# Kernel tuning notes

Hardware: AMD Instinct MI355X
Metric: run time of the kernel (lower is better)

## Reference

```python
import jax, jax.numpy as jnp
import numpy as np

C = 256        # channel
C4 = C // 4    # q/k projection dim
B, NQ, NK = 2, 8192, 8192
BN_EPS = 1e-5


def setup_inputs() -> dict:
    key = jax.random.key(0)
    ks = jax.random.split(key, 8)
    q_tensor = jax.random.normal(ks[0], (B, NQ, C), dtype=jnp.float32)
    kv_tensor = jax.random.normal(ks[1], (B, NK, C), dtype=jnp.float32)
    # 1x1 Conv1d weights == linear layers over the channel dim
    wq = jax.random.normal(ks[2], (C4, C), dtype=jnp.float32) * 0.02
    wk = jax.random.normal(ks[3], (C4, C), dtype=jnp.float32) * 0.02
    wv = jax.random.normal(ks[4], (C, C), dtype=jnp.float32) * 0.02
    wt = jax.random.normal(ks[5], (C, C), dtype=jnp.float32) * 0.02
    bt = jnp.zeros((C,), dtype=jnp.float32)
    # BatchNorm1d (eval mode): affine params + running stats
    gamma = jax.random.uniform(ks[6], (C,), dtype=jnp.float32, minval=0.5, maxval=1.5)
    beta = jax.random.normal(ks[7], (C,), dtype=jnp.float32) * 0.1
    run_mean = jnp.zeros((C,), dtype=jnp.float32)
    run_var = jnp.ones((C,), dtype=jnp.float32)
    return {"q_tensor": q_tensor, "kv_tensor": kv_tensor, "wq": wq, "wk": wk,
            "wv": wv, "wt": wt, "bt": bt, "gamma": gamma, "beta": beta,
            "run_mean": run_mean, "run_var": run_var}


def reference(q_tensor, kv_tensor, wq, wk, wv, wt, bt, gamma, beta, run_mean, run_var):
    # 1x1 conv projections (channel-last form of Conv1d on permuted input)
    x_q = jnp.einsum('bnc,dc->bnd', q_tensor, wq)    # [B, NQ, C4]
    x_k = jnp.einsum('bnc,dc->bnd', kv_tensor, wk)   # [B, NK, C4]
    x_v = jnp.einsum('bnc,dc->bnd', kv_tensor, wv)   # [B, NK, C]
    # unscaled attention: matmul -> softmax -> matmul
    energy = jnp.einsum('bqd,bkd->bqk', x_q, x_k)    # [B, NQ, NK]
    attention = jax.nn.softmax(energy, axis=-1)
    x_r = jnp.einsum('bqk,bkc->bqc', attention, x_v)  # [B, NQ, C]
    # residual difference -> trans conv -> BN (eval) -> ReLU -> residual add
    res = q_tensor - x_r
    y = jnp.einsum('bnc,dc->bnd', res, wt) + bt
    y = (y - run_mean) * jax.lax.rsqrt(run_var + BN_EPS) * gamma + beta
    return jax.nn.relu(y) + q_tensor
```

## Files before the change

### kernel.cpp

```cpp
#include <hip/hip_runtime.h>
#include <hip/hip_bf16.h>

#define DEVINL __device__ __forceinline__

typedef short bf16x8 __attribute__((ext_vector_type(8)));
typedef float f32x4  __attribute__((ext_vector_type(4)));
typedef float f32x16 __attribute__((ext_vector_type(16)));
typedef unsigned int uint2v __attribute__((ext_vector_type(2)));

struct alignas(8) S4 { short x, y, z, w; };

DEVINL short f2bf(float f) {
  __hip_bfloat16 h = __float2bfloat16(f);
  short s; __builtin_memcpy(&s, &h, 2); return s;
}
DEVINL float bf2f(short s) {
  unsigned u = ((unsigned)(unsigned short)s) << 16;
  float f; __builtin_memcpy(&f, &u, 4); return f;
}

DEVINL f32x4 mfma16(bf16x8 a, bf16x8 b, f32x4 c) {
  return __builtin_amdgcn_mfma_f32_16x16x32_bf16(a, b, c, 0, 0, 0);
}
DEVINL f32x16 mfma32(bf16x8 a, bf16x8 b, f32x16 c) {
  return __builtin_amdgcn_mfma_f32_32x32x16_bf16(a, b, c, 0, 0, 0);
}

DEVINL void gld_lds16(const void* gptr, void* lptr) {
  __builtin_amdgcn_global_load_lds(
      (const __attribute__((address_space(1))) unsigned int*)gptr,
      (__attribute__((address_space(3))) unsigned int*)lptr, 16, 0, 0);
}

#define CC 256
#define C4 64
#define BB 2
#define NQ 8192
#define NK 8192
#define NROWS (BB * NQ)
#define DT 10.0f
#define LOG2E 1.44269504f

__global__ void k_setup(const float* __restrict__ wq, const float* __restrict__ wk,
                        const float* __restrict__ wv, const float* __restrict__ wt,
                        const float* __restrict__ bt, const float* __restrict__ gmm,
                        const float* __restrict__ bet, const float* __restrict__ rmean,
                        const float* __restrict__ rvar,
                        short* __restrict__ wqb, short* __restrict__ wkb,
                        short* __restrict__ wvb, short* __restrict__ wtb,
                        float* __restrict__ scale, float* __restrict__ bias) {
  int i = blockIdx.x * 256 + threadIdx.x;
  if (i < C4 * CC) { wqb[i] = f2bf(wq[i] * LOG2E); wkb[i] = f2bf(wk[i]); }
  if (i < CC * CC) { wvb[i] = f2bf(wv[i]); wtb[i] = f2bf(wt[i]); }
  if (i < CC) {
    float s = gmm[i] * rsqrtf(rvar[i] + 1e-5f);
    scale[i] = s;
    bias[i]  = (bt[i] - rmean[i]) * s + bet[i];
  }
}

__global__ __launch_bounds__(256)
void k_projqk(const float* __restrict__ q, const float* __restrict__ kv,
              const short* __restrict__ wqb, const short* __restrict__ wkb,
              short* __restrict__ xq, short* __restrict__ xk) {
  const float* A; const short* W; short* O;
  const bool swz = (blockIdx.y == 1);
  if (!swz) { A = q; W = wqb; O = xq; } else { A = kv; W = wkb; O = xk; }
  const int lane = threadIdx.x & 63, w = threadIdx.x >> 6;
  const int rowbase = blockIdx.x * 128 + w * 32;
  const int lr = lane & 15, lg = lane >> 4;
  f32x4 acc[2][4] = {};
#pragma unroll
  for (int kf = 0; kf < 8; ++kf) {
    bf16x8 a[2];
#pragma unroll
    for (int mf = 0; mf < 2; ++mf) {
      const float* p = A + (size_t)(rowbase + mf * 16 + lr) * CC + kf * 32 + lg * 8;
      float4 x0 = *(const float4*)p, x1 = *(const float4*)(p + 4);
      bf16x8 t;
      t[0] = f2bf(x0.x); t[1] = f2bf(x0.y); t[2] = f2bf(x0.z); t[3] = f2bf(x0.w);
      t[4] = f2bf(x1.x); t[5] = f2bf(x1.y); t[6] = f2bf(x1.z); t[7] = f2bf(x1.w);
      a[mf] = t;
    }
#pragma unroll
    for (int nf = 0; nf < 4; ++nf) {
      bf16x8 b = *(const bf16x8*)(W + (size_t)(nf * 16 + lr) * CC + kf * 32 + lg * 8);
      acc[0][nf] = mfma16(a[0], b, acc[0][nf]);
      acc[1][nf] = mfma16(a[1], b, acc[1][nf]);
    }
  }
#pragma unroll
  for (int mf = 0; mf < 2; ++mf)
#pragma unroll
    for (int nf = 0; nf < 4; ++nf)
#pragma unroll
      for (int r = 0; r < 4; ++r) {
        int row = rowbase + mf * 16 + lg * 4 + r;
        int d = nf * 16 + lr;
        int off = swz ? ((((d >> 3) ^ (row & 7)) << 3) + (d & 7)) : d;
        O[(size_t)row * C4 + off] = f2bf(acc[mf][nf][r]);
      }
}

__global__ __launch_bounds__(256)
void k_projv(const float* __restrict__ kv, const short* __restrict__ wvb,
             short* __restrict__ vt) {
  const int lane = threadIdx.x & 63, w = threadIdx.x >> 6;
  const int rowbase = blockIdx.x * 128 + w * 32;
  const int cb = blockIdx.y * 128;
  const int lr = lane & 15, lg = lane >> 4;
  f32x4 acc[2][8] = {};
#pragma unroll
  for (int kf = 0; kf < 8; ++kf) {
    bf16x8 a[2];
#pragma unroll
    for (int mf = 0; mf < 2; ++mf) {
      const float* p = kv + (size_t)(rowbase + mf * 16 + lr) * CC + kf * 32 + lg * 8;
      float4 x0 = *(const float4*)p, x1 = *(const float4*)(p + 4);
      bf16x8 t;
      t[0] = f2bf(x0.x); t[1] = f2bf(x0.y); t[2] = f2bf(x0.z); t[3] = f2bf(x0.w);
      t[4] = f2bf(x1.x); t[5] = f2bf(x1.y); t[6] = f2bf(x1.z); t[7] = f2bf(x1.w);
      a[mf] = t;
    }
#pragma unroll
    for (int nf = 0; nf < 8; ++nf) {
      bf16x8 b = *(const bf16x8*)(wvb + (size_t)(cb + nf * 16 + lr) * CC + kf * 32 + lg * 8);
      acc[0][nf] = mfma16(a[0], b, acc[0][nf]);
      acc[1][nf] = mfma16(a[1], b, acc[1][nf]);
    }
  }
#pragma unroll
  for (int mf = 0; mf < 2; ++mf) {
    int row = rowbase + mf * 16 + lg * 4;
    int bidx = row >> 13, kib = row & 8191;
    int tile = kib >> 6, kk = kib & 63;
#pragma unroll
    for (int nf = 0; nf < 8; ++nf) {
      int c = cb + nf * 16 + lr;
      S4 st;
      st.x = f2bf(acc[mf][nf][0]); st.y = f2bf(acc[mf][nf][1]);
      st.z = f2bf(acc[mf][nf][2]); st.w = f2bf(acc[mf][nf][3]);
      int off = (((kk >> 3) ^ (c & 7)) << 3) + (kk & 7);
      *(S4*)(vt + (((size_t)bidx * 128 + tile) * CC + c) * 64 + off) = st;
    }
  }
}

__global__ __launch_bounds__(256, 2)
void k_attn(const short* __restrict__ xq, const short* __restrict__ xk,
            const short* __restrict__ vt, float* __restrict__ xr,
            short* __restrict__ po, float* __restrict__ pm,
            float* __restrict__ pl, int nsplit) {
  __shared__ char Lds[40960];
  char* Kt = Lds;
  char* Vt = Lds + 8192;
  const int tid = threadIdx.x;
  const int ln = tid & 63, w = tid >> 6;
  const int qcol = ln & 31, hi = ln >> 5;
  const int b = blockIdx.y, qt = blockIdx.x, kz = blockIdx.z;
  const int kpb = (NK / 64) / nsplit;
  const int kt0 = kz * kpb, kt1 = kt0 + kpb;

  bf16x8 qb[4];
  {
    const short* qrow = xq + (size_t)(b * NQ + qt * 128 + w * 32 + qcol) * C4;
#pragma unroll
    for (int ds = 0; ds < 4; ++ds)
      qb[ds] = *(const bf16x8*)(qrow + ds * 16 + hi * 8);
  }
  f32x16 o[8] = {};
  float m = -1e30f, lsum = 0.f;

  const char* kgbase = (const char*)(xk + (size_t)b * NK * C4);
  const char* vgbase = (const char*)(vt + (size_t)b * 128 * 16384);

  auto stage = [&](int kt) {
    const char* ks = kgbase + (size_t)kt * 8192;
    const char* vs = vgbase + (size_t)kt * 32768;
#pragma unroll
    for (int i = 0; i < 2; ++i)
      gld_lds16(ks + (w * 2 + i) * 1024 + ln * 16, Kt + (w * 2 + i) * 1024);
#pragma unroll
    for (int i = 0; i < 8; ++i)
      gld_lds16(vs + (w * 8 + i) * 1024 + ln * 16, Vt + (w * 8 + i) * 1024);
  };

  stage(kt0);
#pragma unroll 1
  for (int kt = kt0; kt < kt1; ++kt) {
    __syncthreads();
    f32x16 s[2] = {};
#pragma unroll
    for (int kb = 0; kb < 2; ++kb) {
      int key = kb * 32 + qcol;
#pragma unroll
      for (int ds = 0; ds < 4; ++ds) {
        int cc = ds * 2 + hi;
        bf16x8 ka = *(const bf16x8*)(Kt + key * 128 + ((cc ^ (key & 7)) << 4));
        s[kb] = mfma32(ka, qb[ds], s[kb]);
      }
    }
    float pmax = s[0][0];
#pragma unroll
    for (int r = 1; r < 16; ++r) pmax = fmaxf(pmax, s[0][r]);
#pragma unroll
    for (int r = 0; r < 16; ++r) pmax = fmaxf(pmax, s[1][r]);
    pmax = fmaxf(pmax, __shfl_xor(pmax, 32));
    bool grow = pmax > m + DT;
    if (__any(grow)) {
      float alpha = grow ? exp2f(m - pmax) : 1.f;
      m = grow ? pmax : m;
      lsum *= alpha;
#pragma unroll
      for (int cb = 0; cb < 8; ++cb)
#pragma unroll
        for (int r = 0; r < 16; ++r) o[cb][r] *= alpha;
    }
    float rs = 0.f;
#pragma unroll
    for (int r = 0; r < 16; ++r) { float p = exp2f(s[0][r] - m); s[0][r] = p; rs += p; }
#pragma unroll
    for (int r = 0; r < 16; ++r) { float p = exp2f(s[1][r] - m); s[1][r] = p; rs += p; }
    rs += __shfl_xor(rs, 32);
    lsum += rs;
    bf16x8 pb[4];
#pragma unroll
    for (int kb = 0; kb < 2; ++kb) {
      unsigned wv[4], uv[4];
#pragma unroll
      for (int j = 0; j < 4; ++j) {
        asm("v_cvt_pk_bf16_f32 %0, %1, %2"
            : "=v"(wv[j]) : "v"(s[kb][4 * j + 0]), "v"(s[kb][4 * j + 1]));
        asm("v_cvt_pk_bf16_f32 %0, %1, %2"
            : "=v"(uv[j]) : "v"(s[kb][4 * j + 2]), "v"(s[kb][4 * j + 3]));
      }
#pragma unroll
      for (int jj = 0; jj < 2; ++jj) {
        uint2v rw = __builtin_amdgcn_permlane32_swap(wv[2 * jj], wv[2 * jj + 1], false, false);
        uint2v ru = __builtin_amdgcn_permlane32_swap(uv[2 * jj], uv[2 * jj + 1], false, false);
        unsigned tmp[4] = { rw[0], ru[0], rw[1], ru[1] };
        bf16x8 t; __builtin_memcpy(&t, tmp, 16);
        pb[kb * 2 + jj] = t;
      }
    }
#pragma unroll
    for (int cb = 0; cb < 8; ++cb) {
      int c = cb * 32 + qcol;
#pragma unroll
      for (int ks = 0; ks < 4; ++ks) {
        int cc = ks * 2 + hi;
        bf16x8 va = *(const bf16x8*)(Vt + c * 128 + ((cc ^ (c & 7)) << 4));
        o[cb] = mfma32(va, pb[ks], o[cb]);
      }
    }
    __syncthreads();
    if (kt + 1 < kt1) stage(kt + 1);
  }
  char* tb = Lds + w * 4096;
  const size_t rb = (size_t)b * NQ + qt * 128 + w * 32;
  if (nsplit == 1) {
    float inv = 1.f / lsum;
#pragma unroll
    for (int cb = 0; cb < 8; ++cb) {
#pragma unroll
      for (int j = 0; j < 4; ++j) {
        f32x4 v;
        v[0] = o[cb][4 * j + 0] * inv; v[1] = o[cb][4 * j + 1] * inv;
        v[2] = o[cb][4 * j + 2] * inv; v[3] = o[cb][4 * j + 3] * inv;
        *(f32x4*)(tb + qcol * 128 + (((2 * j + hi) ^ (qcol & 7)) << 4)) = v;
      }
#pragma unroll
      for (int jr = 0; jr < 4; ++jr) {
        int qr = jr * 8 + (ln >> 3), cc = ln & 7;
        f32x4 v = *(const f32x4*)(tb + qr * 128 + ((cc ^ (qr & 7)) << 4));
        *(f32x4*)(xr + (rb + qr) * CC + cb * 32 + cc * 4) = v;
      }
    }
  } else {
#pragma unroll
    for (int cb = 0; cb < 8; ++cb) {
#pragma unroll
      for (int j = 0; j < 4; ++j) {
        f32x4 v;
        v[0] = o[cb][4 * j + 0]; v[1] = o[cb][4 * j + 1];
        v[2] = o[cb][4 * j + 2]; v[3] = o[cb][4 * j + 3];
        *(f32x4*)(tb + qcol * 128 + (((2 * j + hi) ^ (qcol & 7)) << 4)) = v;
      }
#pragma unroll
      for (int jr = 0; jr < 4; ++jr) {
        int qr = jr * 8 + (ln >> 3), cc = ln & 7;
        f32x4 v = *(const f32x4*)(tb + qr * 128 + ((cc ^ (qr & 7)) << 4));
        S4 sv; sv.x = f2bf(v[0]); sv.y = f2bf(v[1]); sv.z = f2bf(v[2]); sv.w = f2bf(v[3]);
        *(S4*)(po + ((size_t)kz * NROWS + rb + qr) * CC + cb * 32 + cc * 4) = sv;
      }
    }
    if (ln < 32) {
      size_t g = (size_t)kz * NROWS + rb + qcol;
      pm[g] = m;
      pl[g] = lsum;
    }
  }
}

__global__ __launch_bounds__(256)
void k_combine(const short* __restrict__ po, const float* __restrict__ pm,
               const float* __restrict__ pl, float* __restrict__ xr) {
  int t = blockIdx.x * 256 + threadIdx.x;
  int row = t >> 6, cq = (t & 63) * 4;
  float mi[4], li[4];
#pragma unroll
  for (int i = 0; i < 4; ++i) {
    mi[i] = pm[(size_t)i * NROWS + row];
    li[i] = pl[(size_t)i * NROWS + row];
  }
  float M = fmaxf(fmaxf(mi[0], mi[1]), fmaxf(mi[2], mi[3]));
  float wi[4], L = 0.f;
#pragma unroll
  for (int i = 0; i < 4; ++i) { wi[i] = exp2f(mi[i] - M); L += li[i] * wi[i]; }
  float invL = 1.f / L;
  float a0 = 0, a1 = 0, a2 = 0, a3 = 0;
#pragma unroll
  for (int i = 0; i < 4; ++i) {
    S4 v = *(const S4*)(po + ((size_t)i * NROWS + row) * CC + cq);
    a0 += bf2f(v.x) * wi[i]; a1 += bf2f(v.y) * wi[i];
    a2 += bf2f(v.z) * wi[i]; a3 += bf2f(v.w) * wi[i];
  }
  float4 r; r.x = a0 * invL; r.y = a1 * invL; r.z = a2 * invL; r.w = a3 * invL;
  *(float4*)(xr + (size_t)row * CC + cq) = r;
}

__global__ __launch_bounds__(256)
void k_epilogue(const float* __restrict__ q, const float* __restrict__ xr,
                const short* __restrict__ wtb, const float* __restrict__ scale,
                const float* __restrict__ bias, float* __restrict__ out) {
  const int lane = threadIdx.x & 63, w = threadIdx.x >> 6;
  const int rowbase = blockIdx.x * 128 + w * 32;
  const int cb = blockIdx.y * 128;
  const int lr = lane & 15, lg = lane >> 4;
  f32x4 acc[2][8] = {};
#pragma unroll
  for (int kf = 0; kf < 8; ++kf) {
    bf16x8 a[2];
#pragma unroll
    for (int mf = 0; mf < 2; ++mf) {
      size_t base = (size_t)(rowbase + mf * 16 + lr) * CC + kf * 32 + lg * 8;
      float4 q0 = *(const float4*)(q + base), q1 = *(const float4*)(q + base + 4);
      float4 r0 = *(const float4*)(xr + base), r1 = *(const float4*)(xr + base + 4);
      bf16x8 t;
      t[0] = f2bf(q0.x - r0.x); t[1] = f2bf(q0.y - r0.y);
      t[2] = f2bf(q0.z - r0.z); t[3] = f2bf(q0.w - r0.w);
      t[4] = f2bf(q1.x - r1.x); t[5] = f2bf(q1.y - r1.y);
      t[6] = f2bf(q1.z - r1.z); t[7] = f2bf(q1.w - r1.w);
      a[mf] = t;
    }
#pragma unroll
    for (int nf = 0; nf < 8; ++nf) {
      bf16x8 b = *(const bf16x8*)(wtb + (size_t)(cb + nf * 16 + lr) * CC + kf * 32 + lg * 8);
      acc[0][nf] = mfma16(a[0], b, acc[0][nf]);
      acc[1][nf] = mfma16(a[1], b, acc[1][nf]);
    }
  }
#pragma unroll
  for (int nf = 0; nf < 8; ++nf) {
    int c = cb + nf * 16 + lr;
    float sc = scale[c], bi = bias[c];
#pragma unroll
    for (int mf = 0; mf < 2; ++mf)
#pragma unroll
      for (int r = 0; r < 4; ++r) {
        int row = rowbase + mf * 16 + lg * 4 + r;
        float y = acc[mf][nf][r] * sc + bi;
        y = fmaxf(y, 0.f) + q[(size_t)row * CC + c];
        out[(size_t)row * CC + c] = y;
      }
  }
}

extern "C" void kernel_launch(void* const* d_in, const int* in_sizes, int n_in,
                              void* d_out, int out_size, void* d_ws, size_t ws_size,
                              hipStream_t stream) {
  const float* q     = (const float*)d_in[0];
  const float* kv    = (const float*)d_in[1];
  const float* wq    = (const float*)d_in[2];
  const float* wk    = (const float*)d_in[3];
  const float* wv    = (const float*)d_in[4];
  const float* wt    = (const float*)d_in[5];
  const float* bt    = (const float*)d_in[6];
  const float* gmm   = (const float*)d_in[7];
  const float* bet   = (const float*)d_in[8];
  const float* rmean = (const float*)d_in[9];
  const float* rvar  = (const float*)d_in[10];
  float* out = (float*)d_out;
  char* ws = (char*)d_ws;

  short* wqb  = (short*)(ws + 0);
  short* wkb  = (short*)(ws + 32768);
  short* wvb  = (short*)(ws + 65536);
  short* wtb  = (short*)(ws + 196608);
  float* scale= (float*)(ws + 327680);
  float* bias = (float*)(ws + 328704);
  short* xq   = (short*)(ws + 329728);
  short* xk   = (short*)(ws + 2426880);
  short* vt   = (short*)(ws + 4524032);
  float* xr   = (float*)(ws + 12912640);
  short* po   = (short*)(ws + 29689856);
  float* pm   = (float*)(ws + 63244288);
  float* pl   = (float*)(ws + 63506432);
  const size_t NEED = 63768576;
  const int nsplit = (ws_size >= NEED) ? 4 : 1;

  k_setup<<<256, 256, 0, stream>>>(wq, wk, wv, wt, bt, gmm, bet, rmean, rvar,
                                   wqb, wkb, wvb, wtb, scale, bias);
  k_projqk<<<dim3(128, 2), 256, 0, stream>>>(q, kv, wqb, wkb, xq, xk);
  k_projv<<<dim3(128, 2), 256, 0, stream>>>(kv, wvb, vt);
  k_attn<<<dim3(64, 2, nsplit), 256, 0, stream>>>(xq, xk, vt, xr, po, pm, pl, nsplit);
  if (nsplit > 1)
    k_combine<<<NROWS * 64 / 256, 256, 0, stream>>>(po, pm, pl, xr);
  k_epilogue<<<dim3(128, 2), 256, 0, stream>>>(q, xr, wtb, scale, bias, out);
}
```

Baseline: 182.6 us.

## Double-buffer K/V tiles in attention and halve projection tile heights

The attention kernel gets a second LDS buffer. The next K/V tile is prefetched with async global-to-LDS loads while the current tile is computed, using a partial vmcnt wait instead of a full sync followed by a serial load. This doubles LDS use to 80KB per block, which may cut occupancy below the intended 2 blocks/SM. Separately, the projection and epilogue kernels now use 16-row tiles per wave instead of 32 and twice as many blocks, to give more parallelism at the cost of less weight reuse.

```diff
diff --git a/kernel.cpp b/kernel.cpp
--- a/kernel.cpp
+++ b/kernel.cpp
@@ -67,79 +67,64 @@
   const bool swz = (blockIdx.y == 1);
   if (!swz) { A = q; W = wqb; O = xq; } else { A = kv; W = wkb; O = xk; }
   const int lane = threadIdx.x & 63, w = threadIdx.x >> 6;
-  const int rowbase = blockIdx.x * 128 + w * 32;
+  const int rowbase = blockIdx.x * 64 + w * 16;
   const int lr = lane & 15, lg = lane >> 4;
-  f32x4 acc[2][4] = {};
+  f32x4 acc[4] = {};
 #pragma unroll
   for (int kf = 0; kf < 8; ++kf) {
-    bf16x8 a[2];
-#pragma unroll
-    for (int mf = 0; mf < 2; ++mf) {
-      const float* p = A + (size_t)(rowbase + mf * 16 + lr) * CC + kf * 32 + lg * 8;
-      float4 x0 = *(const float4*)p, x1 = *(const float4*)(p + 4);
-      bf16x8 t;
-      t[0] = f2bf(x0.x); t[1] = f2bf(x0.y); t[2] = f2bf(x0.z); t[3] = f2bf(x0.w);
-      t[4] = f2bf(x1.x); t[5] = f2bf(x1.y); t[6] = f2bf(x1.z); t[7] = f2bf(x1.w);
-      a[mf] = t;
-    }
+    const float* p = A + (size_t)(rowbase + lr) * CC + kf * 32 + lg * 8;
+    float4 x0 = *(const float4*)p, x1 = *(const float4*)(p + 4);
+    bf16x8 a;
+    a[0] = f2bf(x0.x); a[1] = f2bf(x0.y); a[2] = f2bf(x0.z); a[3] = f2bf(x0.w);
+    a[4] = f2bf(x1.x); a[5] = f2bf(x1.y); a[6] = f2bf(x1.z); a[7] = f2bf(x1.w);
 #pragma unroll
     for (int nf = 0; nf < 4; ++nf) {
       bf16x8 b = *(const bf16x8*)(W + (size_t)(nf * 16 + lr) * CC + kf * 32 + lg * 8);
-      acc[0][nf] = mfma16(a[0], b, acc[0][nf]);
-      acc[1][nf] = mfma16(a[1], b, acc[1][nf]);
-    }
-  }
-#pragma unroll
-  for (int mf = 0; mf < 2; ++mf)
-#pragma unroll
-    for (int nf = 0; nf < 4; ++nf)
-#pragma unroll
-      for (int r = 0; r < 4; ++r) {
-        int row = rowbase + mf * 16 + lg * 4 + r;
-        int d = nf * 16 + lr;
-        int off = swz ? ((((d >> 3) ^ (row & 7)) << 3) + (d & 7)) : d;
-        O[(size_t)row * C4 + off] = f2bf(acc[mf][nf][r]);
-      }
+      acc[nf] = mfma16(a, b, acc[nf]);
+    }
+  }
+#pragma unroll
+  for (int nf = 0; nf < 4; ++nf)
+#pragma unroll
+    for (int r = 0; r < 4; ++r) {
+      int row = rowbase + lg * 4 + r;
+      int d = nf * 16 + lr;
+      int off = swz ? ((((d >> 3) ^ (row & 7)) << 3) + (d & 7)) : d;
+      O[(size_t)row * C4 + off] = f2bf(acc[nf][r]);
+    }
 }
 
 __global__ __launch_bounds__(256)
 void k_projv(const float* __restrict__ kv, const short* __restrict__ wvb,
              short* __restrict__ vt) {
   const int lane = threadIdx.x & 63, w = threadIdx.x >> 6;
-  const int rowbase = blockIdx.x * 128 + w * 32;
+  const int rowbase = blockIdx.x * 64 + w * 16;
   const int cb = blockIdx.y * 128;
   const int lr = lane & 15, lg = lane >> 4;
-  f32x4 acc[2][8] = {};
+  f32x4 acc[8] = {};
 #pragma unroll
   for (int kf = 0; kf < 8; ++kf) {
-    bf16x8 a[2];
-#pragma unroll
-    for (int mf = 0; mf < 2; ++mf) {
-      const float* p = kv + (size_t)(rowbase + mf * 16 + lr) * CC + kf * 32 + lg * 8;
-      float4 x0 = *(const float4*)p, x1 = *(const float4*)(p + 4);
-      bf16x8 t;
-      t[0] = f2bf(x0.x); t[1] = f2bf(x0.y); t[2] = f2bf(x0.z); t[3] = f2bf(x0.w);
-      t[4] = f2bf(x1.x); t[5] = f2bf(x1.y); t[6] = f2bf(x1.z); t[7] = f2bf(x1.w);
-      a[mf] = t;
-    }
+    const float* p = kv + (size_t)(rowbase + lr) * CC + kf * 32 + lg * 8;
+    float4 x0 = *(const float4*)p, x1 = *(const float4*)(p + 4);
+    bf16x8 a;
+    a[0] = f2bf(x0.x); a[1] = f2bf(x0.y); a[2] = f2bf(x0.z); a[3] = f2bf(x0.w);
+    a[4] = f2bf(x1.x); a[5] = f2bf(x1.y); a[6] = f2bf(x1.z); a[7] = f2bf(x1.w);
 #pragma unroll
     for (int nf = 0; nf < 8; ++nf) {
       bf16x8 b = *(const bf16x8*)(wvb + (size_t)(cb + nf * 16 + lr) * CC + kf * 32 + lg * 8);
-      acc[0][nf] = mfma16(a[0], b, acc[0][nf]);
-      acc[1][nf] = mfma16(a[1], b, acc[1][nf]);
-    }
-  }
-#pragma unroll
-  for (int mf = 0; mf < 2; ++mf) {
-    int row = rowbase + mf * 16 + lg * 4;
+      acc[nf] = mfma16(a, b, acc[nf]);
+    }
+  }
+  {
+    int row = rowbase + lg * 4;
     int bidx = row >> 13, kib = row & 8191;
     int tile = kib >> 6, kk = kib & 63;
 #pragma unroll
     for (int nf = 0; nf < 8; ++nf) {
       int c = cb + nf * 16 + lr;
       S4 st;
-      st.x = f2bf(acc[mf][nf][0]); st.y = f2bf(acc[mf][nf][1]);
-      st.z = f2bf(acc[mf][nf][2]); st.w = f2bf(acc[mf][nf][3]);
+      st.x = f2bf(acc[nf][0]); st.y = f2bf(acc[nf][1]);
+      st.z = f2bf(acc[nf][2]); st.w = f2bf(acc[nf][3]);
       int off = (((kk >> 3) ^ (c & 7)) << 3) + (kk & 7);
       *(S4*)(vt + (((size_t)bidx * 128 + tile) * CC + c) * 64 + off) = st;
     }
@@ -151,9 +136,7 @@
             const short* __restrict__ vt, float* __restrict__ xr,
             short* __restrict__ po, float* __restrict__ pm,
             float* __restrict__ pl, int nsplit) {
-  __shared__ char Lds[40960];
-  char* Kt = Lds;
-  char* Vt = Lds + 8192;
+  __shared__ char Lds[81920];
   const int tid = threadIdx.x;
   const int ln = tid & 63, w = tid >> 6;
   const int qcol = ln & 31, hi = ln >> 5;
@@ -174,21 +157,30 @@
   const char* kgbase = (const char*)(xk + (size_t)b * NK * C4);
   const char* vgbase = (const char*)(vt + (size_t)b * 128 * 16384);
 
-  auto stage = [&](int kt) {
+  auto stage = [&](int kt, char* base) {
     const char* ks = kgbase + (size_t)kt * 8192;
     const char* vs = vgbase + (size_t)kt * 32768;
 #pragma unroll
     for (int i = 0; i < 2; ++i)
-      gld_lds16(ks + (w * 2 + i) * 1024 + ln * 16, Kt + (w * 2 + i) * 1024);
+      gld_lds16(ks + (w * 2 + i) * 1024 + ln * 16, base + (w * 2 + i) * 1024);
 #pragma unroll
     for (int i = 0; i < 8; ++i)
-      gld_lds16(vs + (w * 8 + i) * 1024 + ln * 16, Vt + (w * 8 + i) * 1024);
+      gld_lds16(vs + (w * 8 + i) * 1024 + ln * 16, base + 8192 + (w * 8 + i) * 1024);
   };
 
-  stage(kt0);
+  stage(kt0, Lds);
 #pragma unroll 1
   for (int kt = kt0; kt < kt1; ++kt) {
-    __syncthreads();
+    char* Kc = Lds + ((kt - kt0) & 1) * 40960;
+    char* Vc = Kc + 8192;
+    if (kt + 1 < kt1) {
+      stage(kt + 1, Lds + ((~(kt - kt0)) & 1) * 40960);
+      asm volatile("s_waitcnt vmcnt(10)" ::: "memory");
+    } else {
+      asm volatile("s_waitcnt vmcnt(0)" ::: "memory");
+    }
+    __builtin_amdgcn_s_barrier();
+    __builtin_amdgcn_sched_barrier(0);
     f32x16 s[2] = {};
 #pragma unroll
     for (int kb = 0; kb < 2; ++kb) {
@@ -196,7 +188,7 @@
 #pragma unroll
       for (int ds = 0; ds < 4; ++ds) {
         int cc = ds * 2 + hi;
-        bf16x8 ka = *(const bf16x8*)(Kt + key * 128 + ((cc ^ (key & 7)) << 4));
+        bf16x8 ka = *(const bf16x8*)(Kc + key * 128 + ((cc ^ (key & 7)) << 4));
         s[kb] = mfma32(ka, qb[ds], s[kb]);
       }
     }
@@ -249,12 +241,13 @@
 #pragma unroll
       for (int ks = 0; ks < 4; ++ks) {
         int cc = ks * 2 + hi;
-        bf16x8 va = *(const bf16x8*)(Vt + c * 128 + ((cc ^ (c & 7)) << 4));
+        bf16x8 va = *(const bf16x8*)(Vc + c * 128 + ((cc ^ (c & 7)) << 4));
         o[cb] = mfma32(va, pb[ks], o[cb]);
       }
     }
-    __syncthreads();
-    if (kt + 1 < kt1) stage(kt + 1);
+    asm volatile("" ::: "memory");
+    __builtin_amdgcn_sched_barrier(0);
+    __builtin_amdgcn_s_barrier();
   }
   char* tb = Lds + w * 4096;
   const size_t rb = (size_t)b * NQ + qt * 128 + w * 32;
@@ -334,30 +327,24 @@
                 const short* __restrict__ wtb, const float* __restrict__ scale,
                 const float* __restrict__ bias, float* __restrict__ out) {
   const int lane = threadIdx.x & 63, w = threadIdx.x >> 6;
-  const int rowbase = blockIdx.x * 128 + w * 32;
+  const int rowbase = blockIdx.x * 64 + w * 16;
   const int cb = blockIdx.y * 128;
   const int lr = lane & 15, lg = lane >> 4;
-  f32x4 acc[2][8] = {};
+  f32x4 acc[8] = {};
 #pragma unroll
   for (int kf = 0; kf < 8; ++kf) {
-    bf16x8 a[2];
-#pragma unroll
-    for (int mf = 0; mf < 2; ++mf) {
-      size_t base = (size_t)(rowbase + mf * 16 + lr) * CC + kf * 32 + lg * 8;
-      float4 q0 = *(const float4*)(q + base), q1 = *(const float4*)(q + base + 4);
-      float4 r0 = *(const float4*)(xr + base), r1 = *(const float4*)(xr + base + 4);
-      bf16x8 t;
-      t[0] = f2bf(q0.x - r0.x); t[1] = f2bf(q0.y - r0.y);
-      t[2] = f2bf(q0.z - r0.z); t[3] = f2bf(q0.w - r0.w);
-      t[4] = f2bf(q1.x - r1.x); t[5] = f2bf(q1.y - r1.y);
-      t[6] = f2bf(q1.z - r1.z); t[7] = f2bf(q1.w - r1.w);
-      a[mf] = t;
-    }
+    size_t base = (size_t)(rowbase + lr) * CC + kf * 32 + lg * 8;
+    float4 q0 = *(const float4*)(q + base), q1 = *(const float4*)(q + base + 4);
+    float4 r0 = *(const float4*)(xr + base), r1 = *(const float4*)(xr + base + 4);
+    bf16x8 a;
+    a[0] = f2bf(q0.x - r0.x); a[1] = f2bf(q0.y - r0.y);
+    a[2] = f2bf(q0.z - r0.z); a[3] = f2bf(q0.w - r0.w);
+    a[4] = f2bf(q1.x - r1.x); a[5] = f2bf(q1.y - r1.y);
+    a[6] = f2bf(q1.z - r1.z); a[7] = f2bf(q1.w - r1.w);
 #pragma unroll
     for (int nf = 0; nf < 8; ++nf) {
       bf16x8 b = *(const bf16x8*)(wtb + (size_t)(cb + nf * 16 + lr) * CC + kf * 32 + lg * 8);
-      acc[0][nf] = mfma16(a[0], b, acc[0][nf]);
-      acc[1][nf] = mfma16(a[1], b, acc[1][nf]);
+      acc[nf] = mfma16(a, b, acc[nf]);
     }
   }
 #pragma unroll
@@ -365,14 +352,12 @@
     int c = cb + nf * 16 + lr;
     float sc = scale[c], bi = bias[c];
 #pragma unroll
-    for (int mf = 0; mf < 2; ++mf)
-#pragma unroll
-      for (int r = 0; r < 4; ++r) {
-        int row = rowbase + mf * 16 + lg * 4 + r;
-        float y = acc[mf][nf][r] * sc + bi;
-        y = fmaxf(y, 0.f) + q[(size_t)row * CC + c];
-        out[(size_t)row * CC + c] = y;
-      }
+    for (int r = 0; r < 4; ++r) {
+      int row = rowbase + lg * 4 + r;
+      float y = acc[nf][r] * sc + bi;
+      y = fmaxf(y, 0.f) + q[(size_t)row * CC + c];
+      out[(size_t)row * CC + c] = y;
+    }
   }
 }
 
@@ -411,10 +396,10 @@
 
   k_setup<<<256, 256, 0, stream>>>(wq, wk, wv, wt, bt, gmm, bet, rmean, rvar,
                                    wqb, wkb, wvb, wtb, scale, bias);
-  k_projqk<<<dim3(128, 2), 256, 0, stream>>>(q, kv, wqb, wkb, xq, xk);
-  k_projv<<<dim3(128, 2), 256, 0, stream>>>(kv, wvb, vt);
+  k_projqk<<<dim3(256, 2), 256, 0, stream>>>(q, kv, wqb, wkb, xq, xk);
+  k_projv<<<dim3(256, 2), 256, 0, stream>>>(kv, wvb, vt);
   k_attn<<<dim3(64, 2, nsplit), 256, 0, stream>>>(xq, xk, vt, xr, po, pm, pl, nsplit);
   if (nsplit > 1)
     k_combine<<<NROWS * 64 / 256, 256, 0, stream>>>(po, pm, pl, xr);
-  k_epilogue<<<dim3(128, 2), 256, 0, stream>>>(q, xr, wtb, scale, bias, out);
-}
+  k_epilogue<<<dim3(256, 2), 256, 0, stream>>>(q, xr, wtb, scale, bias, out);
+}
```

Result: faster. 174.7 us (-4.4%).
